# Optimization experiments

Hardware: AMD Instinct MI355X
Metric: run time of the kernel (lower is better)

## Reference

```python
import jax, jax.numpy as jnp
import numpy as np

N_NODES = 100000
N_EDGES = 1600000
F_IN = 128
HID = 128


def setup_inputs() -> dict:
    key = jax.random.key(0)
    ks = jax.random.split(key, 10)
    x = jax.random.normal(ks[0], (N_NODES, F_IN), dtype=jnp.float32)
    edge_index = jax.random.randint(ks[1], (2, N_EDGES), 0, N_NODES, dtype=jnp.int64)
    edge_weight = jax.random.uniform(ks[2], (N_EDGES,), dtype=jnp.float32)
    # Glorot-style params for the three GCNConv layers (conv_mid reused twice)
    W_in = jax.random.normal(ks[3], (F_IN, HID), dtype=jnp.float32) / np.sqrt(F_IN)
    b_in = jnp.zeros((HID,), dtype=jnp.float32)
    W_mid = jax.random.normal(ks[4], (HID, HID), dtype=jnp.float32) / np.sqrt(HID)
    b_mid = jnp.zeros((HID,), dtype=jnp.float32)
    W_fin = jax.random.normal(ks[5], (HID, 1), dtype=jnp.float32) / np.sqrt(HID)
    b_fin = jnp.zeros((1,), dtype=jnp.float32)
    return {"x": x, "edge_index": edge_index, "edge_weight": edge_weight,
            "W_in": W_in, "b_in": b_in, "W_mid": W_mid, "b_mid": b_mid,
            "W_fin": W_fin, "b_fin": b_fin}


def _gcn_norm(edge_index, edge_weight, n_nodes):
    """PyG GCNConv normalization with implicit self-loops (weight 1).
    Returns (edge_norm [E], self_norm [N]) where self_norm = 1/deg."""
    dst = edge_index[1]
    deg = jax.ops.segment_sum(edge_weight, dst, num_segments=n_nodes) + 1.0
    dinv = jnp.where(deg > 0, jax.lax.rsqrt(deg), 0.0)  # deg^-1/2
    edge_norm = dinv[edge_index[0]] * edge_weight * dinv[dst]
    self_norm = dinv * dinv  # self-loop: dinv[i] * 1 * dinv[i]
    return edge_norm, self_norm


def _gcn_conv(x, edge_index, edge_norm, self_norm, W, b, n_nodes):
    h = x @ W  # [N, out]
    msgs = edge_norm[:, None] * h[edge_index[0]]  # [E, out]
    agg = jax.ops.segment_sum(msgs, edge_index[1], num_segments=n_nodes)
    return agg + self_norm[:, None] * h + b


def reference(x, edge_index, edge_weight, W_in, b_in, W_mid, b_mid, W_fin, b_fin):
    n = x.shape[0]
    edge_norm, self_norm = _gcn_norm(edge_index, edge_weight, n)
    h = jax.nn.relu(_gcn_conv(x, edge_index, edge_norm, self_norm, W_in, b_in, n))
    h = jax.nn.relu(_gcn_conv(h, edge_index, edge_norm, self_norm, W_mid, b_mid, n))
    h = jax.nn.relu(_gcn_conv(h, edge_index, edge_norm, self_norm, W_mid, b_mid, n))
    out = _gcn_conv(h, edge_index, edge_norm, self_norm, W_fin, b_fin, n)
    return out  # [N, 1]
```

## Files before the change

### kernel.cpp

```cpp
#include <hip/hip_runtime.h>
#include <stdint.h>

#define N_NODES 100000
#define N_EDGES 1600000
#define F 128
#define CBN 512
#define NCBK 196
#define CHUNK 4096
#define BUFCAP 10240

typedef _Float16 f16;
typedef _Float16 f16x4 __attribute__((ext_vector_type(4)));
typedef _Float16 f16x8 __attribute__((ext_vector_type(8)));
typedef float f32x4 __attribute__((ext_vector_type(4)));

__device__ inline float unpackw(unsigned int p) {
    unsigned short b = (unsigned short)(p & 0x7FFF);
    return (float)__builtin_bit_cast(f16, b);
}



__launch_bounds__(256)
__global__ void k_binA(const int* __restrict__ ei, const float* __restrict__ w,
                       int* __restrict__ gcur, int2* __restrict__ stage, int e) {
    __shared__ int hist[256];
    __shared__ int bst[257];
    __shared__ int gb[256];
    __shared__ int ls[256];
    __shared__ int rec[CHUNK];
    __shared__ int meta[CHUNK];
    int tid = threadIdx.x;
    int base = blockIdx.x * CHUNK;
    int cnt = min(CHUNK, e - base);
    hist[tid] = 0;
    __syncthreads();

    int ew_[16], mr_[16];
    int nloc = 0;
    if (cnt == CHUNK) {
#pragma unroll
        for (int k = 0; k < 16; k++) {
            int i = base + tid + k * 256;
            int s = ei[i];
            int d = ei[N_EDGES + i];
            f16 hw = (f16)w[i];
            unsigned short wb = __builtin_bit_cast(unsigned short, hw);
            ew_[k] = (int)(((unsigned int)s << 15) | (wb & 0x7FFF));
            int cb = d >> 9;
            int local = d & (CBN - 1);
            int r = atomicAdd(&hist[cb], 1);
            mr_[k] = (cb << 22) | (local << 13) | r;
        }
        nloc = 16;
    } else {
        for (int i = tid; i < cnt; i += 256) {
            int s = ei[base + i];
            int d = ei[N_EDGES + base + i];
            f16 hw = (f16)w[base + i];
            unsigned short wb = __builtin_bit_cast(unsigned short, hw);
            ew_[nloc] = (int)(((unsigned int)s << 15) | (wb & 0x7FFF));
            int cb = d >> 9;
            int local = d & (CBN - 1);
            int r = atomicAdd(&hist[cb], 1);
            mr_[nloc] = (cb << 22) | (local << 13) | r;
            nloc++;
        }
    }
    __syncthreads();
    int v = hist[tid];
    ls[tid] = v;
    __syncthreads();
    for (int off = 1; off < 256; off <<= 1) {
        int t = (tid >= off) ? ls[tid - off] : 0;
        __syncthreads();
        ls[tid] += t;
        __syncthreads();
    }
    bst[tid] = ls[tid] - v;
    if (tid == 255) bst[256] = ls[255];
    __syncthreads();
    for (int k = 0; k < nloc; k++) {
        int m = mr_[k];
        int cb = m >> 22;
        int pos = bst[cb] + (m & 0x1FFF);
        rec[pos] = ew_[k];
        meta[pos] = (cb << 9) | ((m >> 13) & 0x1FF);
    }
    __syncthreads();
    if (tid < NCBK) {
        int c = bst[tid + 1] - bst[tid];
        gb[tid] = c ? atomicAdd(&gcur[tid], c) : 0;
    }
    __syncthreads();
    for (int j = tid; j < cnt; j += 256) {
        int m = meta[j];
        int cb = m >> 9;
        stage[(size_t)cb * BUFCAP + gb[cb] + (j - bst[cb])] = make_int2(m & 511, rec[j]);
    }
}

__launch_bounds__(256)
__global__ void k_binB(const int2* __restrict__ stage, const int* __restrict__ gcur,
                       unsigned int* __restrict__ edges, int2* __restrict__ row2,
                       float* __restrict__ dinv) {
    __shared__ int cnt[CBN];
    __shared__ int ex[CBN + 1];
    __shared__ int cur[CBN];
    __shared__ int ls[256];
    __shared__ unsigned int buf[BUFCAP];
    int tid = threadIdx.x;
    int cb = blockIdx.x;
    int n0 = cb * CBN;
    int nn = min(CBN, N_NODES - n0);
    size_t sbase = (size_t)cb * BUFCAP;
    int ecnt = gcur[cb];
    cnt[tid] = 0;
    cnt[tid + 256] = 0;
    __syncthreads();
    for (int j = tid; j < ecnt; j += 256)
        atomicAdd(&cnt[stage[sbase + j].x], 1);
    __syncthreads();
    int a = cnt[2 * tid], b = cnt[2 * tid + 1];
    int s = a + b;
    ls[tid] = s;
    __syncthreads();
    for (int off = 1; off < 256; off <<= 1) {
        int t = (tid >= off) ? ls[tid - off] : 0;
        __syncthreads();
        ls[tid] += t;
        __syncthreads();
    }
    int bx = ls[tid] - s;
    ex[2 * tid] = bx;
    ex[2 * tid + 1] = bx + a;
    cur[2 * tid] = bx;
    cur[2 * tid + 1] = bx + a;
    if (tid == 255) ex[512] = ls[255];
    __syncthreads();
    for (int l = tid; l < nn; l += 256)
        row2[n0 + l] = make_int2((int)sbase + ex[l], (int)sbase + ex[l + 1]);
    for (int j = tid; j < ecnt; j += 256) {
        int2 r = stage[sbase + j];
        int p = atomicAdd(&cur[r.x], 1);
        buf[p] = (unsigned int)r.y;
    }
    __syncthreads();
    for (int j = tid; j < ecnt; j += 256)
        edges[sbase + j] = buf[j];
    for (int l = tid; l < nn; l += 256) {
        int lo = ex[l];
        int h2 = ex[l + 1];
        float sm = 1.0f;
        for (int j = lo; j < h2; j++) sm += unpackw(buf[j]);
        dinv[n0 + l] = rsqrtf(sm);
    }
}


__global__ void k_wt2(const float* __restrict__ Wa, const float* __restrict__ Wb,
                      f16* __restrict__ Wta, f16* __restrict__ Wtb,
                      int* __restrict__ gcur, unsigned int* __restrict__ edges) {
    int t = threadIdx.x;
    if (blockIdx.x == 2) {
        if (t < NCBK) gcur[t] = 0;
        if (t >= 248) edges[(size_t)NCBK * BUFCAP + (t - 248)] = 0u;
        return;
    }
    const float* W = blockIdx.x ? Wb : Wa;
    f16* Wt = blockIdx.x ? Wtb : Wta;
#pragma unroll
    for (int it = 0; it < 64; it++) {
        int idx = t + it * 256;
        int k = idx >> 7, n = idx & 127;
        Wt[n * 128 + k] = (f16)W[idx];
    }
}


#define LDK 136

__launch_bounds__(256, 2)
__global__ void k_gemmf(const float* __restrict__ A, const f16* __restrict__ Wt,
                        const float* __restrict__ dinv, f16* __restrict__ H, int nrows) {
    __shared__ f16 Ws[128 * LDK];
    int tid = threadIdx.x;
    int r0 = blockIdx.x * 128;
    int wave = tid >> 6;
    int lane = tid & 63;
    int lrow = lane & 15;
    int quad = lane >> 4;

    f16x8 a[2][4];
#pragma unroll
    for (int mt = 0; mt < 2; mt++) {
        int row = r0 + wave * 32 + mt * 16 + lrow;
#pragma unroll
        for (int kc = 0; kc < 4; kc++) {
            if (row < nrows) {
                float4 lo = *(const float4*)&A[(size_t)row * F + kc * 32 + quad * 8];
                float4 hi = *(const float4*)&A[(size_t)row * F + kc * 32 + quad * 8 + 4];
                f16x8 f;
                f[0] = (f16)lo.x; f[1] = (f16)lo.y; f[2] = (f16)lo.z; f[3] = (f16)lo.w;
                f[4] = (f16)hi.x; f[5] = (f16)hi.y; f[6] = (f16)hi.z; f[7] = (f16)hi.w;
                a[mt][kc] = f;
            } else {
                a[mt][kc] = (f16x8){};
            }
        }
    }
#pragma unroll
    for (int it = 0; it < 8; it++) {
        int c = tid + it * 256;
        int rw = c >> 4;
        int off = (c & 15) * 8;
        *(f16x8*)&Ws[rw * LDK + off] = *(const f16x8*)&Wt[rw * 128 + off];
    }
    __syncthreads();

    f32x4 acc[2][8] = {};
#pragma unroll
    for (int kc = 0; kc < 4; kc++) {
        f16x8 b[8];
#pragma unroll
        for (int nt = 0; nt < 8; nt++)
            b[nt] = *(const f16x8*)&Ws[(nt * 16 + lrow) * LDK + kc * 32 + quad * 8];
#pragma unroll
        for (int nt = 0; nt < 8; nt++) {
            acc[0][nt] = __builtin_amdgcn_mfma_f32_16x16x32_f16(a[0][kc], b[nt], acc[0][nt], 0, 0, 0);
            acc[1][nt] = __builtin_amdgcn_mfma_f32_16x16x32_f16(a[1][kc], b[nt], acc[1][nt], 0, 0, 0);
        }
    }
    __syncthreads();
#pragma unroll
    for (int mt = 0; mt < 2; mt++) {
#pragma unroll
        for (int r = 0; r < 4; r++) {
            int lr = wave * 32 + mt * 16 + quad * 4 + r;
            int grow = r0 + lr;
            float dv = (grow < nrows) ? dinv[grow] : 0.f;
#pragma unroll
            for (int nt = 0; nt < 8; nt++)
                Ws[lr * 132 + nt * 16 + lrow] = (f16)(acc[mt][nt][r] * dv);
        }
    }
    __syncthreads();
#pragma unroll
    for (int it = 0; it < 8; it++) {
        int c = it * 256 + tid;
        int rw = c >> 4;
        int col = (c & 15) * 8;
        int grow = r0 + rw;
        if (grow < nrows)
            *(f16x8*)&H[(size_t)grow * F + col] = *(const f16x8*)&Ws[rw * 132 + col];
    }
}

__launch_bounds__(256, 4)
__global__ void k_agg_gemm(const f16* __restrict__ Hin, const int2* __restrict__ row2,
                           const unsigned int* __restrict__ edges,
                           const float* __restrict__ dinv, const float* __restrict__ bias,
                           const f16* __restrict__ Wt, f16* __restrict__ Hout, int nrows) {
    __shared__ f16 S[128 * LDK];
    int tid = threadIdx.x;
    int r0 = blockIdx.x * 128;
    int wave = tid >> 6;
    int lane = tid & 63;
    int sub = lane & 15;
    int quad = lane >> 4;

    float4 b0 = *(const float4*)&bias[sub * 8];
    float4 b1 = *(const float4*)&bias[sub * 8 + 4];
    float bb[8] = {b0.x, b0.y, b0.z, b0.w, b1.x, b1.y, b1.z, b1.w};
    for (int it = 0; it < 8; it++) {
        int l = wave * 32 + it * 4 + quad;
        int node = r0 + l;
        f16x8 o = (f16x8){};
        if (node < nrows) {
            int2 rr = row2[node];
            int beg = rr.x, end = rr.y;
            float acc0[8] = {}, acc1[8] = {}, acc2[8] = {}, acc3[8] = {};
            for (int t = (beg & ~3); t < end; t += 8) {
                uint4 ea = *(const uint4*)&edges[t];
                uint4 eb = *(const uint4*)&edges[t + 4];
                unsigned int e[8] = {ea.x, ea.y, ea.z, ea.w, eb.x, eb.y, eb.z, eb.w};
                float w[8];
                unsigned int srcw[8];
#pragma unroll
                for (int k = 0; k < 8; k++) {
                    bool live = (t + k >= beg) && (t + k < end);
                    w[k] = live ? unpackw(e[k]) : 0.f;
                    srcw[k] = (t + k < end) ? e[k] : ea.x;
                }
                f16x8 v[8];
#pragma unroll
                for (int k = 0; k < 8; k++)
                    v[k] = *(const f16x8*)&Hin[(size_t)(srcw[k] >> 15) * F + sub * 8];
#pragma unroll
                for (int j = 0; j < 8; j++) {
                    acc0[j] = fmaf(w[0], (float)v[0][j], acc0[j]);
                    acc1[j] = fmaf(w[1], (float)v[1][j], acc1[j]);
                    acc2[j] = fmaf(w[2], (float)v[2][j], acc2[j]);
                    acc3[j] = fmaf(w[3], (float)v[3][j], acc3[j]);
                    acc0[j] = fmaf(w[4], (float)v[4][j], acc0[j]);
                    acc1[j] = fmaf(w[5], (float)v[5][j], acc1[j]);
                    acc2[j] = fmaf(w[6], (float)v[6][j], acc2[j]);
                    acc3[j] = fmaf(w[7], (float)v[7][j], acc3[j]);
                }
            }
            float dd = dinv[node];
            f16x8 h = *(const f16x8*)&Hin[(size_t)node * F + sub * 8];
#pragma unroll
            for (int j = 0; j < 8; j++) {
                float a = acc0[j] + acc1[j] + acc2[j] + acc3[j] + (float)h[j];
                o[j] = (f16)fmaxf(fmaf(dd, a, bb[j]), 0.f);
            }
        }
        *(f16x8*)&S[l * LDK + sub * 8] = o;
    }
    __syncthreads();

    f16x8 a[2][4];
#pragma unroll
    for (int mt = 0; mt < 2; mt++) {
        int l = wave * 32 + mt * 16 + sub;
#pragma unroll
        for (int kc = 0; kc < 4; kc++)
            a[mt][kc] = *(const f16x8*)&S[l * LDK + kc * 32 + quad * 8];
    }
    __syncthreads();
#pragma unroll
    for (int it = 0; it < 8; it++) {
        int c = tid + it * 256;
        int rw = c >> 4;
        int off = (c & 15) * 8;
        *(f16x8*)&S[rw * LDK + off] = *(const f16x8*)&Wt[rw * 128 + off];
    }
    __syncthreads();

    f32x4 acc[2][8] = {};
#pragma unroll
    for (int kc = 0; kc < 4; kc++) {
        f16x8 b[8];
#pragma unroll
        for (int nt = 0; nt < 8; nt++)
            b[nt] = *(const f16x8*)&S[(nt * 16 + sub) * LDK + kc * 32 + quad * 8];
#pragma unroll
        for (int nt = 0; nt < 8; nt++) {
            acc[0][nt] = __builtin_amdgcn_mfma_f32_16x16x32_f16(a[0][kc], b[nt], acc[0][nt], 0, 0, 0);
            acc[1][nt] = __builtin_amdgcn_mfma_f32_16x16x32_f16(a[1][kc], b[nt], acc[1][nt], 0, 0, 0);
        }
    }
    __syncthreads();
#pragma unroll
    for (int mt = 0; mt < 2; mt++) {
#pragma unroll
        for (int r = 0; r < 4; r++) {
            int lr = wave * 32 + mt * 16 + quad * 4 + r;
            int grow = r0 + lr;
            float dv = (grow < nrows) ? dinv[grow] : 0.f;
#pragma unroll
            for (int nt = 0; nt < 8; nt++)
                S[lr * 132 + nt * 16 + sub] = (f16)(acc[mt][nt][r] * dv);
        }
    }
    __syncthreads();
#pragma unroll
    for (int it = 0; it < 8; it++) {
        int c = it * 256 + tid;
        int rw = c >> 4;
        int col = (c & 15) * 8;
        int grow = r0 + rw;
        if (grow < nrows)
            *(f16x8*)&Hout[(size_t)grow * F + col] = *(const f16x8*)&S[rw * 132 + col];
    }
}

__launch_bounds__(256)
__global__ void k_agg_dot(const f16* __restrict__ H16, const int2* __restrict__ row2,
                          const unsigned int* __restrict__ edges,
                          const float* __restrict__ dinv, const float* __restrict__ bias,
                          const float* __restrict__ Wf, float* __restrict__ sout, int n) {
    int node = blockIdx.x * 16 + (threadIdx.x >> 4);
    if (node >= n) return;
    int sub = threadIdx.x & 15;
    int2 rr = row2[node];
    int beg = rr.x, end = rr.y;
    float acc0[8] = {}, acc1[8] = {}, acc2[8] = {}, acc3[8] = {};
    for (int t = (beg & ~3); t < end; t += 8) {
        uint4 ea = *(const uint4*)&edges[t];
        uint4 eb = *(const uint4*)&edges[t + 4];
        unsigned int e[8] = {ea.x, ea.y, ea.z, ea.w, eb.x, eb.y, eb.z, eb.w};
        float w[8];
        unsigned int srcw[8];
#pragma unroll
        for (int k = 0; k < 8; k++) {
            bool live = (t + k >= beg) && (t + k < end);
            w[k] = live ? unpackw(e[k]) : 0.f;
            srcw[k] = (t + k < end) ? e[k] : ea.x;
        }
        f16x8 v[8];
#pragma unroll
        for (int k = 0; k < 8; k++)
            v[k] = *(const f16x8*)&H16[(size_t)(srcw[k] >> 15) * F + sub * 8];
#pragma unroll
        for (int j = 0; j < 8; j++) {
            acc0[j] = fmaf(w[0], (float)v[0][j], acc0[j]);
            acc1[j] = fmaf(w[1], (float)v[1][j], acc1[j]);
            acc2[j] = fmaf(w[2], (float)v[2][j], acc2[j]);
            acc3[j] = fmaf(w[3], (float)v[3][j], acc3[j]);
            acc0[j] = fmaf(w[4], (float)v[4][j], acc0[j]);
            acc1[j] = fmaf(w[5], (float)v[5][j], acc1[j]);
            acc2[j] = fmaf(w[6], (float)v[6][j], acc2[j]);
            acc3[j] = fmaf(w[7], (float)v[7][j], acc3[j]);
        }
    }
    float dd = dinv[node];
    f16x8 h = *(const f16x8*)&H16[(size_t)node * F + sub * 8];
    float4 b0 = *(const float4*)&bias[sub * 8];
    float4 b1 = *(const float4*)&bias[sub * 8 + 4];
    float bb[8] = {b0.x, b0.y, b0.z, b0.w, b1.x, b1.y, b1.z, b1.w};
    float4 w0v = *(const float4*)&Wf[sub * 8];
    float4 w1v = *(const float4*)&Wf[sub * 8 + 4];
    float ww[8] = {w0v.x, w0v.y, w0v.z, w0v.w, w1v.x, w1v.y, w1v.z, w1v.w};
    float p = 0.f;
#pragma unroll
    for (int j = 0; j < 8; j++) {
        float a = acc0[j] + acc1[j] + acc2[j] + acc3[j] + (float)h[j];
        p += fmaxf(fmaf(dd, a, bb[j]), 0.f) * ww[j];
    }
    p += __shfl_xor(p, 8, 64);
    p += __shfl_xor(p, 4, 64);
    p += __shfl_xor(p, 2, 64);
    p += __shfl_xor(p, 1, 64);
    if (sub == 0) sout[node] = dd * p;
}

__global__ void k_aggs(const float* __restrict__ s, const int2* __restrict__ row2,
                       const unsigned int* __restrict__ edges,
                       const float* __restrict__ dinv, const float* __restrict__ bf,
                       float* __restrict__ out, int n) {
    int i = blockIdx.x * blockDim.x + threadIdx.x;
    if (i >= n) return;
    float dd = dinv[i];
    float ae = s[i];
    int2 rr = row2[i];
    for (int j = rr.x; j < rr.y; j++) {
        unsigned int p = edges[j];
        ae = fmaf(unpackw(p), s[p >> 15], ae);
    }
    out[i] = fmaf(dd, ae, bf[0]);
}


extern "C" void kernel_launch(void* const* d_in, const int* in_sizes, int n_in,
                              void* d_out, int out_size, void* d_ws, size_t ws_size,
                              hipStream_t stream) {
    const float* x    = (const float*)d_in[0];
    const int*   ei   = (const int*)d_in[1];
    const float* ew   = (const float*)d_in[2];
    const float* Win  = (const float*)d_in[3];
    const float* bin  = (const float*)d_in[4];
    const float* Wmid = (const float*)d_in[5];
    const float* bmid = (const float*)d_in[6];
    const float* Wfin = (const float*)d_in[7];
    const float* bfin = (const float*)d_in[8];
    float* out = (float*)d_out;

    char* ws = (char*)d_ws;
    size_t off = 0;
    auto alloc = [&](size_t bytes) -> char* {
        char* p = ws + off;
        off = (off + bytes + 255) & ~(size_t)255;
        return p;
    };
    float* dinv  = (float*)alloc((size_t)N_NODES * 4);
    int2*  row2  = (int2*)alloc((size_t)N_NODES * 8);
    unsigned int* edges = (unsigned int*)alloc(((size_t)NCBK * BUFCAP + 8) * 4);
    int*   gcur  = (int*)alloc(256 * 4);
    f16*   wtin  = (f16*)alloc(128 * 128 * 2);
    f16*   wtmid = (f16*)alloc(128 * 128 * 2);
    f16*   Ha    = (f16*)alloc((size_t)N_NODES * F * 2);
    f16*   Hb    = (f16*)alloc((size_t)N_NODES * F * 2);
    int2* stage = (int2*)Ha;
    float* sbuf = (float*)Hb;

    dim3 b256(256);
    int gN = (N_NODES + 255) / 256;
    int gW = (N_NODES + 15) / 16;
    int gG = (N_NODES + 127) / 128;
    int gA = (N_EDGES + CHUNK - 1) / CHUNK;

    hipLaunchKernelGGL(k_wt2, dim3(3), b256, 0, stream, Win, Wmid, wtin, wtmid, gcur, edges);
    hipLaunchKernelGGL(k_binA, dim3(gA), b256, 0, stream, ei, ew, gcur, stage, N_EDGES);
    hipLaunchKernelGGL(k_binB, dim3(NCBK), b256, 0, stream, stage, gcur, edges, row2, dinv);

    hipLaunchKernelGGL(k_gemmf, dim3(gG), b256, 0, stream, x, wtin, dinv, Ha, N_NODES);
    hipLaunchKernelGGL(k_agg_gemm, dim3(gG), b256, 0, stream, Ha, row2, edges, dinv, bin, wtmid, Hb, N_NODES);
    hipLaunchKernelGGL(k_agg_gemm, dim3(gG), b256, 0, stream, Hb, row2, edges, dinv, bmid, wtmid, Ha, N_NODES);
    hipLaunchKernelGGL(k_agg_dot, dim3(gW), b256, 0, stream, Ha, row2, edges, dinv, bmid, Wfin, sbuf, N_NODES);
    hipLaunchKernelGGL(k_aggs, dim3(gN), b256, 0, stream, sbuf, row2, edges, dinv, bfin, out, N_NODES);
}
```

Before: 379.2 us.

## Load GEMM B-fragments from global and replace block barriers with wave-local LDS fences

The GEMM kernels no longer stage the f16 weight matrix into LDS. Each wave reads its B fragments straight from global memory (L2/L1-cached). Every wave now writes and reads only its own 32 rows of the shared tile, so the __syncthreads calls become a per-wave lgkmcnt wait plus a scheduling barrier. k_gemmf's occupancy hint is raised to 4 blocks, and the weight transpose kernel now writes Wt contiguously instead of reading W contiguously. This removes block-wide barriers and the LDS copy of W. The cost is repeated global or cache loads of W inside the MFMA loop, and it relies on rows being strictly wave-private.

```diff
diff --git a/kernel.cpp b/kernel.cpp
--- a/kernel.cpp
+++ b/kernel.cpp
@@ -19,6 +19,10 @@
     return (float)__builtin_bit_cast(f16, b);
 }
 
+__device__ inline void lds_fence_wave() {
+    asm volatile("s_waitcnt lgkmcnt(0)" ::: "memory");
+    __builtin_amdgcn_sched_barrier(0);
+}
 
 
 __launch_bounds__(256)
@@ -172,29 +176,29 @@
 #pragma unroll
     for (int it = 0; it < 64; it++) {
         int idx = t + it * 256;
-        int k = idx >> 7, n = idx & 127;
-        Wt[n * 128 + k] = (f16)W[idx];
+        int n = idx >> 7, k = idx & 127;
+        Wt[idx] = (f16)W[k * 128 + n];
     }
 }
 
 
 #define LDK 136
 
-__launch_bounds__(256, 2)
+__launch_bounds__(256, 4)
 __global__ void k_gemmf(const float* __restrict__ A, const f16* __restrict__ Wt,
                         const float* __restrict__ dinv, f16* __restrict__ H, int nrows) {
-    __shared__ f16 Ws[128 * LDK];
+    __shared__ f16 S[128 * LDK];
     int tid = threadIdx.x;
     int r0 = blockIdx.x * 128;
     int wave = tid >> 6;
     int lane = tid & 63;
-    int lrow = lane & 15;
+    int sub = lane & 15;
     int quad = lane >> 4;
 
     f16x8 a[2][4];
 #pragma unroll
     for (int mt = 0; mt < 2; mt++) {
-        int row = r0 + wave * 32 + mt * 16 + lrow;
+        int row = r0 + wave * 32 + mt * 16 + sub;
 #pragma unroll
         for (int kc = 0; kc < 4; kc++) {
             if (row < nrows) {
@@ -209,14 +213,6 @@
             }
         }
     }
-#pragma unroll
-    for (int it = 0; it < 8; it++) {
-        int c = tid + it * 256;
-        int rw = c >> 4;
-        int off = (c & 15) * 8;
-        *(f16x8*)&Ws[rw * LDK + off] = *(const f16x8*)&Wt[rw * 128 + off];
-    }
-    __syncthreads();
 
     f32x4 acc[2][8] = {};
 #pragma unroll
@@ -224,14 +220,13 @@
         f16x8 b[8];
 #pragma unroll
         for (int nt = 0; nt < 8; nt++)
-            b[nt] = *(const f16x8*)&Ws[(nt * 16 + lrow) * LDK + kc * 32 + quad * 8];
+            b[nt] = *(const f16x8*)&Wt[(nt * 16 + sub) * 128 + kc * 32 + quad * 8];
 #pragma unroll
         for (int nt = 0; nt < 8; nt++) {
             acc[0][nt] = __builtin_amdgcn_mfma_f32_16x16x32_f16(a[0][kc], b[nt], acc[0][nt], 0, 0, 0);
             acc[1][nt] = __builtin_amdgcn_mfma_f32_16x16x32_f16(a[1][kc], b[nt], acc[1][nt], 0, 0, 0);
         }
     }
-    __syncthreads();
 #pragma unroll
     for (int mt = 0; mt < 2; mt++) {
 #pragma unroll
@@ -241,18 +236,16 @@
             float dv = (grow < nrows) ? dinv[grow] : 0.f;
 #pragma unroll
             for (int nt = 0; nt < 8; nt++)
-                Ws[lr * 132 + nt * 16 + lrow] = (f16)(acc[mt][nt][r] * dv);
-        }
-    }
-    __syncthreads();
+                S[lr * LDK + nt * 16 + sub] = (f16)(acc[mt][nt][r] * dv);
+        }
+    }
+    lds_fence_wave();
 #pragma unroll
     for (int it = 0; it < 8; it++) {
-        int c = it * 256 + tid;
-        int rw = c >> 4;
-        int col = (c & 15) * 8;
-        int grow = r0 + rw;
+        int lr = wave * 32 + it * 4 + quad;
+        int grow = r0 + lr;
         if (grow < nrows)
-            *(f16x8*)&H[(size_t)grow * F + col] = *(const f16x8*)&Ws[rw * 132 + col];
+            *(f16x8*)&H[(size_t)grow * F + sub * 8] = *(const f16x8*)&S[lr * LDK + sub * 8];
     }
 }
 
@@ -318,7 +311,7 @@
         }
         *(f16x8*)&S[l * LDK + sub * 8] = o;
     }
-    __syncthreads();
+    lds_fence_wave();
 
     f16x8 a[2][4];
 #pragma unroll
@@ -328,15 +321,6 @@
         for (int kc = 0; kc < 4; kc++)
             a[mt][kc] = *(const f16x8*)&S[l * LDK + kc * 32 + quad * 8];
     }
-    __syncthreads();
-#pragma unroll
-    for (int it = 0; it < 8; it++) {
-        int c = tid + it * 256;
-        int rw = c >> 4;
-        int off = (c & 15) * 8;
-        *(f16x8*)&S[rw * LDK + off] = *(const f16x8*)&Wt[rw * 128 + off];
-    }
-    __syncthreads();
 
     f32x4 acc[2][8] = {};
 #pragma unroll
@@ -344,14 +328,13 @@
         f16x8 b[8];
 #pragma unroll
         for (int nt = 0; nt < 8; nt++)
-            b[nt] = *(const f16x8*)&S[(nt * 16 + sub) * LDK + kc * 32 + quad * 8];
+            b[nt] = *(const f16x8*)&Wt[(nt * 16 + sub) * 128 + kc * 32 + quad * 8];
 #pragma unroll
         for (int nt = 0; nt < 8; nt++) {
             acc[0][nt] = __builtin_amdgcn_mfma_f32_16x16x32_f16(a[0][kc], b[nt], acc[0][nt], 0, 0, 0);
             acc[1][nt] = __builtin_amdgcn_mfma_f32_16x16x32_f16(a[1][kc], b[nt], acc[1][nt], 0, 0, 0);
         }
     }
-    __syncthreads();
 #pragma unroll
     for (int mt = 0; mt < 2; mt++) {
 #pragma unroll
@@ -361,18 +344,16 @@
             float dv = (grow < nrows) ? dinv[grow] : 0.f;
 #pragma unroll
             for (int nt = 0; nt < 8; nt++)
-                S[lr * 132 + nt * 16 + sub] = (f16)(acc[mt][nt][r] * dv);
-        }
-    }
-    __syncthreads();
+                S[lr * LDK + nt * 16 + sub] = (f16)(acc[mt][nt][r] * dv);
+        }
+    }
+    lds_fence_wave();
 #pragma unroll
     for (int it = 0; it < 8; it++) {
-        int c = it * 256 + tid;
-        int rw = c >> 4;
-        int col = (c & 15) * 8;
-        int grow = r0 + rw;
+        int lr = wave * 32 + it * 4 + quad;
+        int grow = r0 + lr;
         if (grow < nrows)
-            *(f16x8*)&Hout[(size_t)grow * F + col] = *(const f16x8*)&S[rw * 132 + col];
+            *(f16x8*)&Hout[(size_t)grow * F + sub * 8] = *(const f16x8*)&S[lr * LDK + sub * 8];
     }
 }
 
```

Result: slower. 396.8 us (+4.6%).
